# Optimization experiments

Measured on AMD Instinct MI355X. Metric: run time of the kernel, lower is better.

Reference implementation:

```python
import jax, jax.numpy as jnp
import numpy as np

E, H, FF = 1024, 16, 4096
HD = E // H
B, S = 4, 2048


def _ln(x, g, b, eps=1e-5):
    m = jnp.mean(x, axis=-1, keepdims=True)
    v = jnp.mean((x - m) ** 2, axis=-1, keepdims=True)
    return (x - m) / jnp.sqrt(v + eps) * g + b


def setup_inputs() -> dict:
    k = jax.random.key(0)
    ks = jax.random.split(k, 12)
    sd = 0.02
    return {
        "value": jax.random.normal(ks[0], (B, S, E), jnp.float32),
        "key": jax.random.normal(ks[1], (B, S, E), jnp.float32),
        "query": jax.random.normal(ks[2], (B, S, E), jnp.float32),
        "mask": jnp.ones((B, 1, 1, S), jnp.int32),
        "Wv": sd * jax.random.normal(ks[3], (E, E), jnp.float32),
        "Wk": sd * jax.random.normal(ks[4], (E, E), jnp.float32),
        "Wq": sd * jax.random.normal(ks[5], (E, E), jnp.float32),
        "Wo": sd * jax.random.normal(ks[6], (E, E), jnp.float32),
        "bo": jnp.zeros((E,), jnp.float32),
        "ln1_g": jnp.ones((E,), jnp.float32), "ln1_b": jnp.zeros((E,), jnp.float32),
        "ln2_g": jnp.ones((E,), jnp.float32), "ln2_b": jnp.zeros((E,), jnp.float32),
        "lnf_g": jnp.ones((E,), jnp.float32), "lnf_b": jnp.zeros((E,), jnp.float32),
        "W1": sd * jax.random.normal(ks[7], (E, FF), jnp.float32),
        "b1": jnp.zeros((FF,), jnp.float32),
        "W2": sd * jax.random.normal(ks[8], (FF, E), jnp.float32),
        "b2": jnp.zeros((E,), jnp.float32),
    }


def reference(value, key, query, mask, Wv, Wk, Wq, Wo, bo,
              ln1_g, ln1_b, ln2_g, ln2_b, lnf_g, lnf_b, W1, b1, W2, b2):
    N, Sq, Em = query.shape
    # pre-norms (value & key share prenorm2 params, as in the torch module)
    v = _ln(value, ln2_g, ln2_b)
    k = _ln(key, ln2_g, ln2_b)
    q = _ln(query, ln1_g, ln1_b)
    # QKV projections (no bias), split heads
    V = (v @ Wv).reshape(N, v.shape[1], H, HD)
    K = (k @ Wk).reshape(N, k.shape[1], H, HD)
    Q = (q @ Wq).reshape(N, Sq, H, HD)
    energy = jnp.einsum("nqhd,nkhd->nhqk", Q, K)  # [N,H,Sq,Sk]
    energy = jnp.where(mask == 0, jnp.float32(-1e20), energy)
    attn = jax.nn.softmax(energy / jnp.float32(HD ** 0.5), axis=-1)
    out = jnp.einsum("nhqk,nkhd->nqhd", attn, V).reshape(N, Sq, Em)
    out = out @ Wo + bo
    x = out + q  # residual (drop_path is identity in eval)
    f = _ln(x, lnf_g, lnf_b) @ W1 + b1
    f = jax.nn.gelu(f, approximate=False) @ W2 + b2
    return f + x
```

## Files before the change

kernel.cpp:

```cpp
#include <hip/hip_runtime.h>
#include <hip/hip_bf16.h>
#include <math.h>

typedef __bf16 bf16x8 __attribute__((ext_vector_type(8)));
typedef __bf16 bf16x4 __attribute__((ext_vector_type(4)));
typedef float f32x4 __attribute__((ext_vector_type(4)));

#define AS1 __attribute__((address_space(1)))
#define AS3 __attribute__((address_space(3)))

__device__ __forceinline__ void gll16(const __bf16* g, __bf16* l) {
    __builtin_amdgcn_global_load_lds((const AS1 unsigned int*)g,
                                     (AS3 unsigned int*)l, 16, 0, 0);
}

__device__ __forceinline__ unsigned pkbf(float a, float b) {
    union { __bf16 h[2]; unsigned u; } t;
    t.h[0] = (__bf16)a; t.h[1] = (__bf16)b;
    return t.u;
}

__global__ __launch_bounds__(256) void transpose_all(
    const float* __restrict__ Wq, const float* __restrict__ Wk,
    const float* __restrict__ Wv, const float* __restrict__ Wo,
    const float* __restrict__ W1, const float* __restrict__ W2,
    __bf16* __restrict__ Wqt, __bf16* __restrict__ Wkt,
    __bf16* __restrict__ Wvt, __bf16* __restrict__ Wot,
    __bf16* __restrict__ W1t, __bf16* __restrict__ W2t) {
    int g = blockIdx.x;
    const float* W; __bf16* Wt; int K, N, kt, nt;
    if (g < 4096) {
        int mi = g >> 10, loc = g & 1023;
        K = 1024; N = 1024; kt = loc >> 5; nt = loc & 31;
        W  = mi == 0 ? Wq  : mi == 1 ? Wk  : mi == 2 ? Wv  : Wo;
        Wt = mi == 0 ? Wqt : mi == 1 ? Wkt : mi == 2 ? Wvt : Wot;
    } else if (g < 8192) {
        int loc = g - 4096; W = W1; Wt = W1t;
        K = 1024; N = 4096; kt = loc >> 7; nt = loc & 127;
    } else {
        int loc = g - 8192; W = W2; Wt = W2t;
        K = 4096; N = 1024; kt = loc >> 5; nt = loc & 31;
    }
    int k0 = kt * 32, n0 = nt * 32;
    __shared__ float tile[32][33];
    int tx = threadIdx.x & 31, ty = threadIdx.x >> 5;
    #pragma unroll
    for (int j = ty; j < 32; j += 8)
        tile[j][tx] = W[(size_t)(k0 + j) * N + n0 + tx];
    __syncthreads();
    #pragma unroll
    for (int j = ty; j < 32; j += 8)
        Wt[(size_t)(n0 + j) * K + k0 + tx] = (__bf16)tile[tx][j];
}

__global__ __launch_bounds__(256) void ln3_kernel(
    const float* __restrict__ q, const float* __restrict__ k,
    const float* __restrict__ v,
    const float* __restrict__ g1, const float* __restrict__ b1,
    const float* __restrict__ g2, const float* __restrict__ b2,
    float* __restrict__ qln, __bf16* __restrict__ qbf,
    __bf16* __restrict__ kbf, __bf16* __restrict__ vbf) {
    const int E = 1024;
    int which = blockIdx.y;
    const float* x = which == 0 ? q : which == 1 ? k : v;
    const float* g = which == 0 ? g1 : g2;
    const float* bb = which == 0 ? b1 : b2;
    float* o32 = which == 0 ? qln : nullptr;
    __bf16* obf = which == 0 ? qbf : which == 1 ? kbf : vbf;

    size_t row = blockIdx.x;
    int t = threadIdx.x;
    float4 val = ((const float4*)(x + row * E))[t];
    float s  = val.x + val.y + val.z + val.w;
    float s2 = val.x * val.x + val.y * val.y + val.z * val.z + val.w * val.w;
    #pragma unroll
    for (int off = 32; off >= 1; off >>= 1) {
        s  += __shfl_down(s, off);
        s2 += __shfl_down(s2, off);
    }
    __shared__ float red[2][4];
    int wid = t >> 6, lane = t & 63;
    if (lane == 0) { red[0][wid] = s; red[1][wid] = s2; }
    __syncthreads();
    if (t == 0) {
        float S1 = red[0][0] + red[0][1] + red[0][2] + red[0][3];
        float S2 = red[1][0] + red[1][1] + red[1][2] + red[1][3];
        float mean = S1 / E;
        float var  = S2 / E - mean * mean;
        red[0][0] = mean;
        red[1][0] = 1.0f / sqrtf(var + 1e-5f);
    }
    __syncthreads();
    float mean = red[0][0], rstd = red[1][0];
    float4 gv = ((const float4*)g)[t];
    float4 bv = ((const float4*)bb)[t];
    float y0 = (val.x - mean) * rstd * gv.x + bv.x;
    float y1 = (val.y - mean) * rstd * gv.y + bv.y;
    float y2 = (val.z - mean) * rstd * gv.z + bv.z;
    float y3 = (val.w - mean) * rstd * gv.w + bv.w;
    if (o32) ((float4*)(o32 + row * E))[t] = make_float4(y0, y1, y2, y3);
    bf16x4 o;
    o[0] = (__bf16)y0; o[1] = (__bf16)y1; o[2] = (__bf16)y2; o[3] = (__bf16)y3;
    ((bf16x4*)(obf + row * E))[t] = o;
}

__global__ __launch_bounds__(256) void ln_kernel(const float* __restrict__ x,
                                                 const float* __restrict__ g,
                                                 const float* __restrict__ bb,
                                                 __bf16* __restrict__ outbf) {
    const int E = 1024;
    size_t row = blockIdx.x;
    int t = threadIdx.x;
    float4 v = ((const float4*)(x + row * E))[t];
    float s  = v.x + v.y + v.z + v.w;
    float s2 = v.x * v.x + v.y * v.y + v.z * v.z + v.w * v.w;
    #pragma unroll
    for (int off = 32; off >= 1; off >>= 1) {
        s  += __shfl_down(s, off);
        s2 += __shfl_down(s2, off);
    }
    __shared__ float red[2][4];
    int wid = t >> 6, lane = t & 63;
    if (lane == 0) { red[0][wid] = s; red[1][wid] = s2; }
    __syncthreads();
    if (t == 0) {
        float S1 = red[0][0] + red[0][1] + red[0][2] + red[0][3];
        float S2 = red[1][0] + red[1][1] + red[1][2] + red[1][3];
        float mean = S1 / E;
        float var  = S2 / E - mean * mean;
        red[0][0] = mean;
        red[1][0] = 1.0f / sqrtf(var + 1e-5f);
    }
    __syncthreads();
    float mean = red[0][0], rstd = red[1][0];
    float4 gv = ((const float4*)g)[t];
    float4 bv = ((const float4*)bb)[t];
    bf16x4 o;
    o[0] = (__bf16)((v.x - mean) * rstd * gv.x + bv.x);
    o[1] = (__bf16)((v.y - mean) * rstd * gv.y + bv.y);
    o[2] = (__bf16)((v.z - mean) * rstd * gv.z + bv.z);
    o[3] = (__bf16)((v.w - mean) * rstd * gv.w + bv.w);
    ((bf16x4*)(outbf + row * E))[t] = o;
}

template <int EPI, int TMD, int TND>
__global__ __launch_bounds__(256) void gemm_tn(const __bf16* __restrict__ A,
                                               const __bf16* __restrict__ Bt,
                                               const float* __restrict__ bias,
                                               const float* __restrict__ resid,
                                               void* __restrict__ Cout,
                                               int M, int N, int K) {
    __shared__ __bf16 As[TMD * 32 * 64];
    __shared__ __bf16 Bs[TND * 32 * 64];
    int tid  = threadIdx.x;
    int lane = tid & 63, wid = tid >> 6;
    int quad = lane >> 4, l15 = lane & 15;
    int waveM = wid >> 1, waveN = wid & 1;
    size_t rowBase = (size_t)blockIdx.y * (TMD * 32);
    size_t colBase = (size_t)blockIdx.x * (TND * 32);

    int lrow8  = lane >> 3;
    int lchunk = (lane & 7) ^ lrow8;
    const __bf16* Ag0 = A  + (rowBase + wid * (8 * TMD) + lrow8) * (size_t)K + lchunk * 8;
    const __bf16* Bg0 = Bt + (colBase + wid * (8 * TND) + lrow8) * (size_t)K + lchunk * 8;
    __bf16* AsB = &As[(wid * 8 * TMD) * 64];
    __bf16* BsB = &Bs[(wid * 8 * TND) * 64];

    f32x4 acc[TMD][TND] = {};
    int swz = l15 & 7;

    for (int kb = 0; kb < K; kb += 64) {
        __syncthreads();
        #pragma unroll
        for (int i = 0; i < TMD; i++)
            gll16(Ag0 + (size_t)i * 8 * K + kb, AsB + i * 512);
        #pragma unroll
        for (int i = 0; i < TND; i++)
            gll16(Bg0 + (size_t)i * 8 * K + kb, BsB + i * 512);
        __syncthreads();
        #pragma unroll
        for (int ks = 0; ks < 2; ks++) {
            int p = ((ks * 4 + quad) ^ swz) * 8;
            bf16x8 af[TMD], bfr[TND];
            #pragma unroll
            for (int mi = 0; mi < TMD; mi++)
                af[mi] = *(const bf16x8*)&As[(waveM * 16 * TMD + mi * 16 + l15) * 64 + p];
            #pragma unroll
            for (int ni = 0; ni < TND; ni++)
                bfr[ni] = *(const bf16x8*)&Bs[(waveN * 16 * TND + ni * 16 + l15) * 64 + p];
            #pragma unroll
            for (int mi = 0; mi < TMD; mi++)
                #pragma unroll
                for (int ni = 0; ni < TND; ni++)
                    acc[mi][ni] = __builtin_amdgcn_mfma_f32_16x16x32_bf16(
                        bfr[ni], af[mi], acc[mi][ni], 0, 0, 0);
        }
    }

    #pragma unroll
    for (int mi = 0; mi < TMD; mi++)
    #pragma unroll
    for (int ni = 0; ni < TND; ni++) {
        size_t row = rowBase + waveM * 16 * TMD + mi * 16 + l15;
        size_t col = colBase + waveN * 16 * TND + ni * 16 + quad * 4;
        f32x4 v = acc[mi][ni];
        if (EPI == 1) {
            float4 b4 = *(const float4*)&bias[col];
            float4 r4 = *(const float4*)&resid[row * N + col];
            float4 o;
            o.x = v[0] + b4.x + r4.x; o.y = v[1] + b4.y + r4.y;
            o.z = v[2] + b4.z + r4.z; o.w = v[3] + b4.w + r4.w;
            *(float4*)&((float*)Cout)[row * N + col] = o;
        } else {
            float4 b4 = *(const float4*)&bias[col];
            bf16x4 pk;
            #pragma unroll
            for (int r = 0; r < 4; r++) {
                float t2 = v[r] + ((const float*)&b4)[r];
                pk[r] = (__bf16)(0.5f * t2 * (1.0f + erff(t2 * 0.70710678118654752f)));
            }
            *(bf16x4*)&((__bf16*)Cout)[row * N + col] = pk;
        }
    }
}

__global__ __launch_bounds__(256) void gemm_qkv(const __bf16* __restrict__ qbf,
                                                const __bf16* __restrict__ kbf,
                                                const __bf16* __restrict__ vbf,
                                                const __bf16* __restrict__ Wqt,
                                                const __bf16* __restrict__ Wkt,
                                                const __bf16* __restrict__ Wvt,
                                                __bf16* __restrict__ QKb,
                                                __bf16* __restrict__ Vtg,
                                                int M, int K) {
    __shared__ __bf16 As[128 * 64];
    __shared__ __bf16 Bs[128 * 64];
    int tid  = threadIdx.x;
    int lane = tid & 63, wid = tid >> 6;
    int quad = lane >> 4, l15 = lane & 15;
    int waveM = wid >> 1, waveN = wid & 1;
    size_t rowBase = (size_t)blockIdx.y * 128;
    int seg = blockIdx.x >> 3;
    size_t colLoc = (size_t)(blockIdx.x & 7) * 128;

    const __bf16* Ap = seg == 0 ? qbf : seg == 1 ? kbf : vbf;
    const __bf16* Bp = seg == 0 ? Wqt : seg == 1 ? Wkt : Wvt;

    int lrow8  = lane >> 3;
    int lchunk = (lane & 7) ^ lrow8;
    const __bf16* Ag0 = Ap + (rowBase + wid * 32 + lrow8) * (size_t)K + lchunk * 8;
    const __bf16* Bg0 = Bp + (colLoc  + wid * 32 + lrow8) * (size_t)K + lchunk * 8;
    __bf16* AsB = &As[(wid * 32) * 64];
    __bf16* BsB = &Bs[(wid * 32) * 64];

    f32x4 acc[4][4] = {};
    int swz = l15 & 7;

    for (int kb = 0; kb < K; kb += 64) {
        __syncthreads();
        #pragma unroll
        for (int i = 0; i < 4; i++) {
            gll16(Ag0 + (size_t)i * 8 * K + kb, AsB + i * 512);
            gll16(Bg0 + (size_t)i * 8 * K + kb, BsB + i * 512);
        }
        __syncthreads();
        #pragma unroll
        for (int ks = 0; ks < 2; ks++) {
            int p = ((ks * 4 + quad) ^ swz) * 8;
            bf16x8 af[4], bfr[4];
            #pragma unroll
            for (int mi = 0; mi < 4; mi++)
                af[mi] = *(const bf16x8*)&As[(waveM * 64 + mi * 16 + l15) * 64 + p];
            #pragma unroll
            for (int ni = 0; ni < 4; ni++)
                bfr[ni] = *(const bf16x8*)&Bs[(waveN * 64 + ni * 16 + l15) * 64 + p];
            if (seg != 2) {
                #pragma unroll
                for (int mi = 0; mi < 4; mi++)
                    #pragma unroll
                    for (int ni = 0; ni < 4; ni++)
                        acc[mi][ni] = __builtin_amdgcn_mfma_f32_16x16x32_bf16(
                            bfr[ni], af[mi], acc[mi][ni], 0, 0, 0);
            } else {
                #pragma unroll
                for (int mi = 0; mi < 4; mi++)
                    #pragma unroll
                    for (int ni = 0; ni < 4; ni++)
                        acc[mi][ni] = __builtin_amdgcn_mfma_f32_16x16x32_bf16(
                            af[mi], bfr[ni], acc[mi][ni], 0, 0, 0);
            }
        }
    }

    if (seg != 2) {
        float sc = seg == 0 ? 0.125f : 1.0f;
        #pragma unroll
        for (int mi = 0; mi < 4; mi++)
        #pragma unroll
        for (int ni = 0; ni < 4; ni++) {
            size_t row = rowBase + waveM * 64 + mi * 16 + l15;
            size_t col = (size_t)seg * 1024 + colLoc + waveN * 64 + ni * 16 + quad * 4;
            bf16x4 pk;
            #pragma unroll
            for (int r = 0; r < 4; r++) pk[r] = (__bf16)(acc[mi][ni][r] * sc);
            *(bf16x4*)&QKb[row * 2048 + col] = pk;
        }
    } else {
        #pragma unroll
        for (int mi = 0; mi < 4; mi++)
        #pragma unroll
        for (int ni = 0; ni < 4; ni++) {
            size_t col = colLoc + waveN * 64 + ni * 16 + l15;
            size_t m0  = rowBase + waveM * 64 + mi * 16 + quad * 4;
            bf16x4 pk;
            #pragma unroll
            for (int r = 0; r < 4; r++) pk[r] = (__bf16)acc[mi][ni][r];
            *(bf16x4*)&Vtg[col * M + m0] = pk;
        }
    }
}

__global__ __launch_bounds__(512, 6) void attn_kernel(const __bf16* __restrict__ QK,
                                                      const __bf16* __restrict__ Vt,
                                                      const int* __restrict__ mask,
                                                      __bf16* __restrict__ Out) {
    const int S = 2048, E = 1024, E2 = 2048, M = 8192;
    int qt = blockIdx.x, bh = blockIdx.y;
    int b = bh >> 4, h = bh & 15;
    int q0 = qt * 128;
    int tid = threadIdx.x, lane = tid & 63, wid = tid >> 6;
    int quad = lane >> 4, l15 = lane & 15;

    __shared__ __bf16 KV[2][2 * 4096];

    bf16x8 aq[2];
    #pragma unroll
    for (int hh = 0; hh < 2; hh++) {
        size_t row = (size_t)(b * S + q0 + wid * 16 + l15);
        aq[hh] = *(const bf16x8*)(QK + row * E2 + h * 64 + hh * 32 + quad * 8);
    }

    int lrow8  = lane >> 3;
    int lchunk = (lane & 7) ^ lrow8;
    const __bf16* Kg0 = QK + (size_t)(b * S + wid * 8 + lrow8) * E2 + 1024 + h * 64 + lchunk * 8;
    const __bf16* Vg0 = Vt + (size_t)(h * 64 + wid * 8 + lrow8) * M + b * S + lchunk * 8;

    int srcA = ((quad & 1) * 2) * 16 + l15;
    int srcB = srcA + 16;
    bool selHi = (quad >= 2);
    int swz = l15 & 7;

    f32x4 accO[4] = {};
    float accl = 0.f;

    gll16(Kg0, &KV[0][wid * 512]);
    gll16(Vg0, &KV[0][4096 + wid * 512]);
    __syncthreads();

    for (int kt = 0; kt < S / 64; kt++) {
        int k0 = kt * 64;
        int buf = kt & 1;
        if (kt + 1 < S / 64) {
            int kn = k0 + 64;
            gll16(Kg0 + (size_t)kn * E2, &KV[buf ^ 1][wid * 512]);
            gll16(Vg0 + kn,              &KV[buf ^ 1][4096 + wid * 512]);
        }
        const __bf16* Ksb = &KV[buf][0];
        const __bf16* Vsb = &KV[buf][4096];

        f32x4 sa[4];
        #pragma unroll
        for (int nt = 0; nt < 4; nt++) {
            bf16x8 a0 = *(const bf16x8*)&Ksb[(nt * 16 + l15) * 64 + ((quad) ^ swz) * 8];
            bf16x8 a1 = *(const bf16x8*)&Ksb[(nt * 16 + l15) * 64 + ((4 + quad) ^ swz) * 8];
            f32x4 a = {};
            a = __builtin_amdgcn_mfma_f32_16x16x32_bf16(a0, aq[0], a, 0, 0, 0);
            a = __builtin_amdgcn_mfma_f32_16x16x32_bf16(a1, aq[1], a, 0, 0, 0);
            sa[nt] = a;
        }

        unsigned pd[4][2];
        #pragma unroll
        for (int nt = 0; nt < 4; nt++) {
            int4 mz = *(const int4*)&mask[b * S + k0 + nt * 16 + quad * 4];
            float p0 = mz.x ? __expf(sa[nt][0]) : 0.f;
            float p1 = mz.y ? __expf(sa[nt][1]) : 0.f;
            float p2 = mz.z ? __expf(sa[nt][2]) : 0.f;
            float p3 = mz.w ? __expf(sa[nt][3]) : 0.f;
            accl += (p0 + p1) + (p2 + p3);
            pd[nt][0] = pkbf(p0, p1);
            pd[nt][1] = pkbf(p2, p3);
        }

        bf16x8 bfrag[2];
        #pragma unroll
        for (int hh = 0; hh < 2; hh++) {
            int ntLo = 2 * hh;
            unsigned dA0 = __shfl((int)pd[ntLo][0], srcA, 64);
            unsigned dB0 = __shfl((int)pd[ntLo + 1][0], srcA, 64);
            unsigned dA1 = __shfl((int)pd[ntLo][1], srcA, 64);
            unsigned dB1 = __shfl((int)pd[ntLo + 1][1], srcA, 64);
            unsigned dA2 = __shfl((int)pd[ntLo][0], srcB, 64);
            unsigned dB2 = __shfl((int)pd[ntLo + 1][0], srcB, 64);
            unsigned dA3 = __shfl((int)pd[ntLo][1], srcB, 64);
            unsigned dB3 = __shfl((int)pd[ntLo + 1][1], srcB, 64);
            union { unsigned u[4]; bf16x8 v; } w;
            w.u[0] = selHi ? dB0 : dA0;
            w.u[1] = selHi ? dB1 : dA1;
            w.u[2] = selHi ? dB2 : dA2;
            w.u[3] = selHi ? dB3 : dA3;
            bfrag[hh] = w.v;
        }

        #pragma unroll
        for (int dt = 0; dt < 4; dt++) {
            bf16x8 v0 = *(const bf16x8*)&Vsb[(dt * 16 + l15) * 64 + ((quad) ^ swz) * 8];
            bf16x8 v1 = *(const bf16x8*)&Vsb[(dt * 16 + l15) * 64 + ((4 + quad) ^ swz) * 8];
            accO[dt] = __builtin_amdgcn_mfma_f32_16x16x32_bf16(v0, bfrag[0], accO[dt], 0, 0, 0);
            accO[dt] = __builtin_amdgcn_mfma_f32_16x16x32_bf16(v1, bfrag[1], accO[dt], 0, 0, 0);
        }
        __syncthreads();
    }

    float l = accl;
    l += __shfl_xor(l, 16, 64);
    l += __shfl_xor(l, 32, 64);
    float inv = 1.0f / l;

    #pragma unroll
    for (int dt = 0; dt < 4; dt++) {
        size_t row = (size_t)(b * S + q0 + wid * 16 + l15);
        bf16x4 pk;
        #pragma unroll
        for (int r = 0; r < 4; r++) pk[r] = (__bf16)(accO[dt][r] * inv);
        *(bf16x4*)&Out[row * E + h * 64 + dt * 16 + quad * 4] = pk;
    }
}

extern "C" void kernel_launch(void* const* d_in, const int* in_sizes, int n_in,
                              void* d_out, int out_size, void* d_ws, size_t ws_size,
                              hipStream_t stream) {
    const int Bb = 4, S = 2048, E = 1024, FF = 4096;
    const int M = Bb * S;

    const float* value = (const float*)d_in[0];
    const float* key   = (const float*)d_in[1];
    const float* query = (const float*)d_in[2];
    const int*   mask  = (const int*)d_in[3];
    const float* Wv    = (const float*)d_in[4];
    const float* Wk    = (const float*)d_in[5];
    const float* Wq    = (const float*)d_in[6];
    const float* Wo    = (const float*)d_in[7];
    const float* bo    = (const float*)d_in[8];
    const float* ln1_g = (const float*)d_in[9];
    const float* ln1_b = (const float*)d_in[10];
    const float* ln2_g = (const float*)d_in[11];
    const float* ln2_b = (const float*)d_in[12];
    const float* lnf_g = (const float*)d_in[13];
    const float* lnf_b = (const float*)d_in[14];
    const float* W1    = (const float*)d_in[15];
    const float* b1    = (const float*)d_in[16];
    const float* W2    = (const float*)d_in[17];
    const float* b2    = (const float*)d_in[18];

    char* ws = (char*)d_ws;
    const size_t MB = 1024 * 1024;
    __bf16* Wqt = (__bf16*)(ws + 0 * MB);
    __bf16* Wkt = (__bf16*)(ws + 2 * MB);
    __bf16* Wvt = (__bf16*)(ws + 4 * MB);
    __bf16* Wot = (__bf16*)(ws + 6 * MB);
    __bf16* W1t = (__bf16*)(ws + 8 * MB);
    __bf16* W2t = (__bf16*)(ws + 16 * MB);
    __bf16* q_bf = (__bf16*)(ws + 24 * MB);
    __bf16* k_bf = (__bf16*)(ws + 40 * MB);
    __bf16* v_bf = (__bf16*)(ws + 56 * MB);
    __bf16* QKb  = (__bf16*)(ws + 72 * MB);
    __bf16* Vtg  = (__bf16*)(ws + 104 * MB);
    __bf16* attn = q_bf;
    __bf16* x_ln = k_bf;
    __bf16* h1   = v_bf;
    float*  qln  = (float*)(ws + 120 * MB);
    float*  x32  = (float*)(ws + 152 * MB);

    transpose_all<<<12288, 256, 0, stream>>>(Wq, Wk, Wv, Wo, W1, W2,
                                             Wqt, Wkt, Wvt, Wot, W1t, W2t);

    ln3_kernel<<<dim3(M, 3), 256, 0, stream>>>(query, key, value,
                                               ln1_g, ln1_b, ln2_g, ln2_b,
                                               qln, q_bf, k_bf, v_bf);

    gemm_qkv<<<dim3(24, M / 128), 256, 0, stream>>>(q_bf, k_bf, v_bf,
                                                    Wqt, Wkt, Wvt, QKb, Vtg, M, E);

    attn_kernel<<<dim3(S / 128, Bb * 16), 512, 0, stream>>>(QKb, Vtg, mask, attn);

    gemm_tn<1, 4, 2><<<dim3(E / 64, M / 128), 256, 0, stream>>>(
        attn, Wot, bo, qln, x32, M, E, E);

    ln_kernel<<<M, 256, 0, stream>>>(x32, lnf_g, lnf_b, x_ln);

    gemm_tn<2, 4, 4><<<dim3(FF / 128, M / 128), 256, 0, stream>>>(
        x_ln, W1t, b1, nullptr, h1, M, FF, E);
    gemm_tn<1, 4, 2><<<dim3(E / 64, M / 128), 256, 0, stream>>>(
        h1, W2t, b2, x32, (float*)d_out, M, E, FF);
}
```

Before: 759.0 us.

## Unify GEMMs on 128x128 tiles with grouped block swizzle; split V projection

Replaces the templated GEMM and the fused QKV kernel with one 128x128-tile GEMM that maps a 1D grid through a group-of-8 row swizzle, so neighbouring blocks share B tiles in L2. The output and W2 projections move from 128x64 to 128x128 tiles, which halves their block count and raises per-block reuse. Q/K projection runs through the generic kernel with a split pointer, and V projection gets its own transposed-output kernel. The cost is fewer blocks for the N=1024 GEMMs (512 blocks), which may leave CUs underused, plus an extra launch.

```diff
diff --git a/kernel.cpp b/kernel.cpp
--- a/kernel.cpp
+++ b/kernel.cpp
@@ -143,66 +143,77 @@
     ((bf16x4*)(outbf + row * E))[t] = o;
 }
 
-template <int EPI, int TMD, int TND>
-__global__ __launch_bounds__(256) void gemm_tn(const __bf16* __restrict__ A,
+template <int EPI>
+__global__ __launch_bounds__(256) void gemm128(const __bf16* __restrict__ A,
+                                               const __bf16* __restrict__ A2,
                                                const __bf16* __restrict__ Bt,
+                                               const __bf16* __restrict__ Bt2,
                                                const float* __restrict__ bias,
                                                const float* __restrict__ resid,
                                                void* __restrict__ Cout,
-                                               int M, int N, int K) {
-    __shared__ __bf16 As[TMD * 32 * 64];
-    __shared__ __bf16 Bs[TND * 32 * 64];
+                                               int M, int N, int K,
+                                               int splitN, float scale) {
+    __shared__ __bf16 As[128 * 64];
+    __shared__ __bf16 Bs[128 * 64];
     int tid  = threadIdx.x;
     int lane = tid & 63, wid = tid >> 6;
     int quad = lane >> 4, l15 = lane & 15;
     int waveM = wid >> 1, waveN = wid & 1;
-    size_t rowBase = (size_t)blockIdx.y * (TMD * 32);
-    size_t colBase = (size_t)blockIdx.x * (TND * 32);
+
+    int GX = N >> 7;
+    int id = blockIdx.x;
+    int x8 = id & 7, t = id >> 3;
+    size_t rowBase = (size_t)((t / GX) * 8 + x8) * 128;
+    size_t colBase = (size_t)(t % GX) * 128;
+
+    const __bf16* Ap = A; const __bf16* Bp = Bt;
+    size_t colLoc = colBase;
+    float sc = scale;
+    if ((int)colBase >= splitN) { Ap = A2; Bp = Bt2; colLoc = colBase - splitN; sc = 1.0f; }
 
     int lrow8  = lane >> 3;
     int lchunk = (lane & 7) ^ lrow8;
-    const __bf16* Ag0 = A  + (rowBase + wid * (8 * TMD) + lrow8) * (size_t)K + lchunk * 8;
-    const __bf16* Bg0 = Bt + (colBase + wid * (8 * TND) + lrow8) * (size_t)K + lchunk * 8;
-    __bf16* AsB = &As[(wid * 8 * TMD) * 64];
-    __bf16* BsB = &Bs[(wid * 8 * TND) * 64];
-
-    f32x4 acc[TMD][TND] = {};
+    const __bf16* Ag0 = Ap + (rowBase + wid * 32 + lrow8) * (size_t)K + lchunk * 8;
+    const __bf16* Bg0 = Bp + (colLoc  + wid * 32 + lrow8) * (size_t)K + lchunk * 8;
+    __bf16* AsB = &As[(wid * 32) * 64];
+    __bf16* BsB = &Bs[(wid * 32) * 64];
+
+    f32x4 acc[4][4] = {};
     int swz = l15 & 7;
 
     for (int kb = 0; kb < K; kb += 64) {
         __syncthreads();
         #pragma unroll
-        for (int i = 0; i < TMD; i++)
+        for (int i = 0; i < 4; i++) {
             gll16(Ag0 + (size_t)i * 8 * K + kb, AsB + i * 512);
-        #pragma unroll
-        for (int i = 0; i < TND; i++)
             gll16(Bg0 + (size_t)i * 8 * K + kb, BsB + i * 512);
+        }
         __syncthreads();
         #pragma unroll
         for (int ks = 0; ks < 2; ks++) {
             int p = ((ks * 4 + quad) ^ swz) * 8;
-            bf16x8 af[TMD], bfr[TND];
-            #pragma unroll
-            for (int mi = 0; mi < TMD; mi++)
-                af[mi] = *(const bf16x8*)&As[(waveM * 16 * TMD + mi * 16 + l15) * 64 + p];
-            #pragma unroll
-            for (int ni = 0; ni < TND; ni++)
-                bfr[ni] = *(const bf16x8*)&Bs[(waveN * 16 * TND + ni * 16 + l15) * 64 + p];
-            #pragma unroll
-            for (int mi = 0; mi < TMD; mi++)
+            bf16x8 af[4], bfr[4];
+            #pragma unroll
+            for (int mi = 0; mi < 4; mi++)
+                af[mi] = *(const bf16x8*)&As[(waveM * 64 + mi * 16 + l15) * 64 + p];
+            #pragma unroll
+            for (int ni = 0; ni < 4; ni++)
+                bfr[ni] = *(const bf16x8*)&Bs[(waveN * 64 + ni * 16 + l15) * 64 + p];
+            #pragma unroll
+            for (int mi = 0; mi < 4; mi++)
                 #pragma unroll
-                for (int ni = 0; ni < TND; ni++)
+                for (int ni = 0; ni < 4; ni++)
                     acc[mi][ni] = __builtin_amdgcn_mfma_f32_16x16x32_bf16(
                         bfr[ni], af[mi], acc[mi][ni], 0, 0, 0);
         }
     }
 
     #pragma unroll
-    for (int mi = 0; mi < TMD; mi++)
-    #pragma unroll
-    for (int ni = 0; ni < TND; ni++) {
-        size_t row = rowBase + waveM * 16 * TMD + mi * 16 + l15;
-        size_t col = colBase + waveN * 16 * TND + ni * 16 + quad * 4;
+    for (int mi = 0; mi < 4; mi++)
+    #pragma unroll
+    for (int ni = 0; ni < 4; ni++) {
+        size_t row = rowBase + waveM * 64 + mi * 16 + l15;
+        size_t col = colBase + waveN * 64 + ni * 16 + quad * 4;
         f32x4 v = acc[mi][ni];
         if (EPI == 1) {
             float4 b4 = *(const float4*)&bias[col];
@@ -211,7 +222,7 @@
             o.x = v[0] + b4.x + r4.x; o.y = v[1] + b4.y + r4.y;
             o.z = v[2] + b4.z + r4.z; o.w = v[3] + b4.w + r4.w;
             *(float4*)&((float*)Cout)[row * N + col] = o;
-        } else {
+        } else if (EPI == 2) {
             float4 b4 = *(const float4*)&bias[col];
             bf16x4 pk;
             #pragma unroll
@@ -220,36 +231,36 @@
                 pk[r] = (__bf16)(0.5f * t2 * (1.0f + erff(t2 * 0.70710678118654752f)));
             }
             *(bf16x4*)&((__bf16*)Cout)[row * N + col] = pk;
-        }
-    }
-}
-
-__global__ __launch_bounds__(256) void gemm_qkv(const __bf16* __restrict__ qbf,
-                                                const __bf16* __restrict__ kbf,
-                                                const __bf16* __restrict__ vbf,
-                                                const __bf16* __restrict__ Wqt,
-                                                const __bf16* __restrict__ Wkt,
-                                                const __bf16* __restrict__ Wvt,
-                                                __bf16* __restrict__ QKb,
-                                                __bf16* __restrict__ Vtg,
-                                                int M, int K) {
+        } else {
+            bf16x4 pk;
+            #pragma unroll
+            for (int r = 0; r < 4; r++) pk[r] = (__bf16)(v[r] * sc);
+            *(bf16x4*)&((__bf16*)Cout)[row * N + col] = pk;
+        }
+    }
+}
+
+__global__ __launch_bounds__(256) void gemmV(const __bf16* __restrict__ A,
+                                             const __bf16* __restrict__ Bt,
+                                             __bf16* __restrict__ Cout,
+                                             int M, int N, int K) {
     __shared__ __bf16 As[128 * 64];
     __shared__ __bf16 Bs[128 * 64];
     int tid  = threadIdx.x;
     int lane = tid & 63, wid = tid >> 6;
     int quad = lane >> 4, l15 = lane & 15;
     int waveM = wid >> 1, waveN = wid & 1;
-    size_t rowBase = (size_t)blockIdx.y * 128;
-    int seg = blockIdx.x >> 3;
-    size_t colLoc = (size_t)(blockIdx.x & 7) * 128;
-
-    const __bf16* Ap = seg == 0 ? qbf : seg == 1 ? kbf : vbf;
-    const __bf16* Bp = seg == 0 ? Wqt : seg == 1 ? Wkt : Wvt;
+
+    int GX = N >> 7;
+    int id = blockIdx.x;
+    int x8 = id & 7, t = id >> 3;
+    size_t rowBase = (size_t)((t / GX) * 8 + x8) * 128;
+    size_t colBase = (size_t)(t % GX) * 128;
 
     int lrow8  = lane >> 3;
     int lchunk = (lane & 7) ^ lrow8;
-    const __bf16* Ag0 = Ap + (rowBase + wid * 32 + lrow8) * (size_t)K + lchunk * 8;
-    const __bf16* Bg0 = Bp + (colLoc  + wid * 32 + lrow8) * (size_t)K + lchunk * 8;
+    const __bf16* Ag0 = A  + (rowBase + wid * 32 + lrow8) * (size_t)K + lchunk * 8;
+    const __bf16* Bg0 = Bt + (colBase + wid * 32 + lrow8) * (size_t)K + lchunk * 8;
     __bf16* AsB = &As[(wid * 32) * 64];
     __bf16* BsB = &Bs[(wid * 32) * 64];
 
@@ -274,49 +285,25 @@
             #pragma unroll
             for (int ni = 0; ni < 4; ni++)
                 bfr[ni] = *(const bf16x8*)&Bs[(waveN * 64 + ni * 16 + l15) * 64 + p];
-            if (seg != 2) {
+            #pragma unroll
+            for (int mi = 0; mi < 4; mi++)
                 #pragma unroll
-                for (int mi = 0; mi < 4; mi++)
-                    #pragma unroll
-                    for (int ni = 0; ni < 4; ni++)
-                        acc[mi][ni] = __builtin_amdgcn_mfma_f32_16x16x32_bf16(
-                            bfr[ni], af[mi], acc[mi][ni], 0, 0, 0);
-            } else {
-                #pragma unroll
-                for (int mi = 0; mi < 4; mi++)
-                    #pragma unroll
-                    for (int ni = 0; ni < 4; ni++)
-                        acc[mi][ni] = __builtin_amdgcn_mfma_f32_16x16x32_bf16(
-                            af[mi], bfr[ni], acc[mi][ni], 0, 0, 0);
-            }
-        }
-    }
-
-    if (seg != 2) {
-        float sc = seg == 0 ? 0.125f : 1.0f;
-        #pragma unroll
-        for (int mi = 0; mi < 4; mi++)
-        #pragma unroll
-        for (int ni = 0; ni < 4; ni++) {
-            size_t row = rowBase + waveM * 64 + mi * 16 + l15;
-            size_t col = (size_t)seg * 1024 + colLoc + waveN * 64 + ni * 16 + quad * 4;
-            bf16x4 pk;
-            #pragma unroll
-            for (int r = 0; r < 4; r++) pk[r] = (__bf16)(acc[mi][ni][r] * sc);
-            *(bf16x4*)&QKb[row * 2048 + col] = pk;
-        }
-    } else {
-        #pragma unroll
-        for (int mi = 0; mi < 4; mi++)
-        #pragma unroll
-        for (int ni = 0; ni < 4; ni++) {
-            size_t col = colLoc + waveN * 64 + ni * 16 + l15;
-            size_t m0  = rowBase + waveM * 64 + mi * 16 + quad * 4;
-            bf16x4 pk;
-            #pragma unroll
-            for (int r = 0; r < 4; r++) pk[r] = (__bf16)acc[mi][ni][r];
-            *(bf16x4*)&Vtg[col * M + m0] = pk;
-        }
+                for (int ni = 0; ni < 4; ni++)
+                    acc[mi][ni] = __builtin_amdgcn_mfma_f32_16x16x32_bf16(
+                        af[mi], bfr[ni], acc[mi][ni], 0, 0, 0);
+        }
+    }
+
+    #pragma unroll
+    for (int mi = 0; mi < 4; mi++)
+    #pragma unroll
+    for (int ni = 0; ni < 4; ni++) {
+        size_t col = colBase + waveN * 64 + ni * 16 + l15;
+        size_t m0  = rowBase + waveM * 64 + mi * 16 + quad * 4;
+        bf16x4 pk;
+        #pragma unroll
+        for (int r = 0; r < 4; r++) pk[r] = (__bf16)acc[mi][ni][r];
+        *(bf16x4*)&Cout[col * M + m0] = pk;
     }
 }
 
@@ -489,18 +476,20 @@
                                                ln1_g, ln1_b, ln2_g, ln2_b,
                                                qln, q_bf, k_bf, v_bf);
 
-    gemm_qkv<<<dim3(24, M / 128), 256, 0, stream>>>(q_bf, k_bf, v_bf,
-                                                    Wqt, Wkt, Wvt, QKb, Vtg, M, E);
+    gemm128<0><<<16 * 64, 256, 0, stream>>>(
+        q_bf, k_bf, Wqt, Wkt, nullptr, nullptr, QKb, M, 2 * E, E, E, 0.125f);
+
+    gemmV<<<8 * 64, 256, 0, stream>>>(v_bf, Wvt, Vtg, M, E, E);
 
     attn_kernel<<<dim3(S / 128, Bb * 16), 512, 0, stream>>>(QKb, Vtg, mask, attn);
 
-    gemm_tn<1, 4, 2><<<dim3(E / 64, M / 128), 256, 0, stream>>>(
-        attn, Wot, bo, qln, x32, M, E, E);
+    gemm128<1><<<8 * 64, 256, 0, stream>>>(
+        attn, attn, Wot, Wot, bo, qln, x32, M, E, E, E, 1.0f);
 
     ln_kernel<<<M, 256, 0, stream>>>(x32, lnf_g, lnf_b, x_ln);
 
-    gemm_tn<2, 4, 4><<<dim3(FF / 128, M / 128), 256, 0, stream>>>(
-        x_ln, W1t, b1, nullptr, h1, M, FF, E);
-    gemm_tn<1, 4, 2><<<dim3(E / 64, M / 128), 256, 0, stream>>>(
-        h1, W2t, b2, x32, (float*)d_out, M, E, FF);
-}
+    gemm128<2><<<32 * 64, 256, 0, stream>>>(
+        x_ln, x_ln, W1t, W1t, b1, nullptr, h1, M, FF, E, FF, 1.0f);
+    gemm128<1><<<8 * 64, 256, 0, stream>>>(
+        h1, h1, W2t, W2t, b2, x32, (float*)d_out, M, E, FF, E, 1.0f);
+}
```

After: 666.4 us. -12.2%, faster.
